# Kernel tuning notes

Hardware: AMD Instinct MI355X
Metric: run time of the kernel (lower is better)

## Reference

```python
import jax, jax.numpy as jnp
import numpy as np

B, T, D = 4, 2048, 1024

def setup_inputs() -> dict:
    key = jax.random.key(0)
    kx, kq, kk, kv = jax.random.split(key, 4)
    lim = 1.0 / np.sqrt(D)
    x = jax.random.normal(kx, (B, T, D), dtype=jnp.float32)
    # nn.Linear weights (stored as [out,in]); applied as x @ W.T
    W_q = jax.random.uniform(kq, (D, D), jnp.float32, -lim, lim)
    W_k = jax.random.uniform(kk, (D, D), jnp.float32, -lim, lim)
    W_v = jax.random.uniform(kv, (D, D), jnp.float32, -lim, lim)
    return {"x": x, "W_q": W_q, "W_k": W_k, "W_v": W_v}

def reference(x, W_q, W_k, W_v):
    d = x.shape[-1]
    Q = jnp.einsum('btd,ed->bte', x, W_q)
    K = jnp.einsum('btd,ed->bte', x, W_k)
    V = jnp.einsum('btd,ed->bte', x, W_v)
    att = jnp.einsum('bqd,bkd->bqk', Q, K) / jnp.sqrt(jnp.asarray(d, x.dtype))
    weights = jax.nn.softmax(att, axis=-1)  # NOTE: original applies no causal mask
    return jnp.einsum('bqk,bkd->bqd', weights, V)
```

## Files before the change

kernel.cpp:

```cpp
#include <hip/hip_runtime.h>
#include <hip/hip_bf16.h>
#include <math.h>
#include <type_traits>


typedef short shortx8 __attribute__((ext_vector_type(8)));
typedef short shortx4 __attribute__((ext_vector_type(4)));
typedef float floatx16 __attribute__((ext_vector_type(16)));
typedef __attribute__((address_space(3))) void lds_void_t;
typedef __attribute__((address_space(1))) const void gmem_void_t;

#define GLD16(gp, lp) \
    __builtin_amdgcn_global_load_lds((gmem_void_t*)(gp), (lds_void_t*)(lp), 16, 0, 0)

#define MODE_PROJ 0
#define MODE_EXP  1
#define MODE_DIV  2

template <int MODE>
__global__ __launch_bounds__(512) void mfma_gemm_abt(
    const __hip_bfloat16* __restrict__ A, const __hip_bfloat16* __restrict__ B,
    void* __restrict__ Cv, float* __restrict__ rowsum,
    __hip_bfloat16* __restrict__ Vt,
    int M, int N, int K, long sA, long sB, long sC, float alpha)
{
    __shared__ __hip_bfloat16 As[256 * 64];
    __shared__ __hip_bfloat16 Bs[128 * 64];

    using CT = std::conditional_t<MODE == MODE_DIV, float, __hip_bfloat16>;

    const int z = blockIdx.z;
    A += (long)z * sA;
    B += (long)z * sB;
    CT* C = (CT*)Cv + (long)z * sC;

    const int t     = threadIdx.x;
    const int wave  = t >> 6;
    const int lane  = t & 63;
    const int m0    = blockIdx.x * 256;
    const int n0    = blockIdx.y * 128;
    const int wm    = (wave >> 1) * 64;
    const int wn    = (wave & 1) * 64;
    const int lrow  = lane & 31;
    const int lhalf = lane >> 5;

    const int srow = t >> 3;
    const int scol = (((t & 7) ^ ((t >> 3) & 7))) * 8;

    const int fr = lrow & 7;

    floatx16 acc[2][2] = {};

    for (int k0 = 0; k0 < K; k0 += 64) {
        #pragma unroll
        for (int q = 0; q < 4; ++q)
            GLD16(A + (long)(m0 + 64 * q + srow) * K + k0 + scol,
                  As + q * 4096 + wave * 512);
        #pragma unroll
        for (int q = 0; q < 2; ++q)
            GLD16(B + (long)(n0 + 64 * q + srow) * K + k0 + scol,
                  Bs + q * 4096 + wave * 512);
        __syncthreads();

        #pragma unroll
        for (int h = 0; h < 4; ++h) {
            const int koff = ((2 * h + lhalf) ^ fr) * 8;
            shortx8 af[2], bf[2];
            #pragma unroll
            for (int i = 0; i < 2; ++i)
                af[i] = *(const shortx8*)(As + (wm + 32 * i + lrow) * 64 + koff);
            #pragma unroll
            for (int j = 0; j < 2; ++j)
                bf[j] = *(const shortx8*)(Bs + (wn + 32 * j + lrow) * 64 + koff);
            #pragma unroll
            for (int i = 0; i < 2; ++i)
                #pragma unroll
                for (int j = 0; j < 2; ++j)
                    acc[i][j] = __builtin_amdgcn_mfma_f32_32x32x16_bf16(
                        af[i], bf[j], acc[i][j], 0, 0, 0);
        }
        __syncthreads();
    }

    if constexpr (MODE == MODE_PROJ) {
        if (z == 2) {
            const int bz   = m0 >> 11;
            const long bo  = (long)bz * N * 2048;
            #pragma unroll
            for (int i = 0; i < 2; ++i)
                #pragma unroll
                for (int j = 0; j < 2; ++j)
                    #pragma unroll
                    for (int g = 0; g < 4; ++g) {
                        const int trow = (m0 + wm + 32 * i + g * 8 + 4 * lhalf) & 2047;
                        const long col = n0 + wn + 32 * j + lrow;
                        shortx4 pk;
                        #pragma unroll
                        for (int r = 0; r < 4; ++r) {
                            __hip_bfloat16 hb = __float2bfloat16(acc[i][j][4 * g + r]);
                            pk[r] = *(short*)&hb;
                        }
                        *(shortx4*)(Vt + bo + col * 2048 + trow) = pk;
                    }
        } else {
            #pragma unroll
            for (int i = 0; i < 2; ++i)
                #pragma unroll
                for (int j = 0; j < 2; ++j)
                    #pragma unroll
                    for (int g = 0; g < 4; ++g)
                        #pragma unroll
                        for (int r = 0; r < 4; ++r) {
                            const long row = m0 + wm + 32 * i + g * 8 + 4 * lhalf + r;
                            const long col = n0 + wn + 32 * j + lrow;
                            C[row * N + col] = __float2bfloat16(acc[i][j][4 * g + r]);
                        }
        }
    } else if constexpr (MODE == MODE_EXP) {
        #pragma unroll
        for (int i = 0; i < 2; ++i) {
            float rs[16];
            #pragma unroll
            for (int reg = 0; reg < 16; ++reg) rs[reg] = 0.0f;
            #pragma unroll
            for (int j = 0; j < 2; ++j)
                #pragma unroll
                for (int g = 0; g < 4; ++g)
                    #pragma unroll
                    for (int r = 0; r < 4; ++r) {
                        const long row = m0 + wm + 32 * i + g * 8 + 4 * lhalf + r;
                        const long col = n0 + wn + 32 * j + lrow;
                        const float e = __expf(acc[i][j][4 * g + r] * alpha);
                        rs[4 * g + r] += e;
                        C[row * N + col] = __float2bfloat16(e);
                    }
            #pragma unroll
            for (int reg = 0; reg < 16; ++reg) {
                float v = rs[reg];
                v += __shfl_xor(v, 1);
                v += __shfl_xor(v, 2);
                v += __shfl_xor(v, 4);
                v += __shfl_xor(v, 8);
                v += __shfl_xor(v, 16);
                if (lrow == 0) {
                    const long row = m0 + wm + 32 * i + (reg >> 2) * 8 + 4 * lhalf + (reg & 3);
                    atomicAdd(&rowsum[(long)z * M + row], v);
                }
            }
        }
    } else {
        #pragma unroll
        for (int i = 0; i < 2; ++i) {
            float inv[16];
            #pragma unroll
            for (int g = 0; g < 4; ++g)
                #pragma unroll
                for (int r = 0; r < 4; ++r) {
                    const long row = m0 + wm + 32 * i + g * 8 + 4 * lhalf + r;
                    inv[4 * g + r] = 1.0f / rowsum[(long)z * M + row];
                }
            #pragma unroll
            for (int j = 0; j < 2; ++j)
                #pragma unroll
                for (int g = 0; g < 4; ++g)
                    #pragma unroll
                    for (int r = 0; r < 4; ++r) {
                        const long row = m0 + wm + 32 * i + g * 8 + 4 * lhalf + r;
                        const long col = n0 + wn + 32 * j + lrow;
                        C[row * N + col] = acc[i][j][4 * g + r] * inv[4 * g + r];
                    }
        }
    }
}

__global__ __launch_bounds__(256) void prep(
    const float* __restrict__ x,
    const float* __restrict__ W0, const float* __restrict__ W1,
    const float* __restrict__ W2,
    __hip_bfloat16* __restrict__ xb, __hip_bfloat16* __restrict__ Wb,
    float* __restrict__ rowsum, int n4x, int n4w)
{
    const long i = (long)blockIdx.x * 256 + threadIdx.x;
    if (i < 2048) {
        float4 zz; zz.x = zz.y = zz.z = zz.w = 0.0f;
        ((float4*)rowsum)[i] = zz;
    }
    const float* src;
    __hip_bfloat16* dst;
    long j;
    if (i < n4x) {
        src = x; dst = xb; j = i;
    } else {
        const long k = i - n4x;
        const int w  = (int)(k >> 18);
        j = k & (n4w - 1);
        src = (w == 0) ? W0 : (w == 1) ? W1 : W2;
        dst = Wb + (long)w * n4w * 4;
    }
    const float4 f = ((const float4*)src)[j];
    dst[j * 4 + 0] = __float2bfloat16(f.x);
    dst[j * 4 + 1] = __float2bfloat16(f.y);
    dst[j * 4 + 2] = __float2bfloat16(f.z);
    dst[j * 4 + 3] = __float2bfloat16(f.w);
}

extern "C" void kernel_launch(void* const* d_in, const int* in_sizes, int n_in,
                              void* d_out, int out_size, void* d_ws, size_t ws_size,
                              hipStream_t stream)
{
    constexpr int  Bb = 4, T = 2048, D = 1024;
    constexpr int  M  = Bb * T;
    constexpr long TD = (long)T * D;
    constexpr long TT = (long)T * T;
    constexpr long MD = (long)M * D;

    const float* x  = (const float*)d_in[0];
    const float* Wq = (const float*)d_in[1];
    const float* Wk = (const float*)d_in[2];
    const float* Wv = (const float*)d_in[3];
    float* out = (float*)d_out;

    __hip_bfloat16* Q  = (__hip_bfloat16*)d_ws;
    __hip_bfloat16* Kb = Q + MD;
    __hip_bfloat16* Vt = Kb + MD;
    __hip_bfloat16* P  = Vt + MD;
    __hip_bfloat16* xb = P + (long)Bb * TT;
    __hip_bfloat16* Wb = xb + MD;
    float*     rowsum  = (float*)(Wb + 3L * D * D);

    constexpr int n4x = (int)(MD / 4);
    constexpr int n4w = D * D / 4;
    prep<<<dim3((n4x + 3 * n4w) / 256), dim3(256), 0, stream>>>(
        x, Wq, Wk, Wv, xb, Wb, rowsum, n4x, n4w);

    dim3 blk(512);

    mfma_gemm_abt<MODE_PROJ><<<dim3(M / 256, D / 128, 3), blk, 0, stream>>>(
        xb, Wb, Q, nullptr, Vt, M, D, D, 0, (long)D * D, MD, 1.0f);

    mfma_gemm_abt<MODE_EXP><<<dim3(T / 256, T / 128, Bb), blk, 0, stream>>>(
        Q, Kb, P, rowsum, nullptr, T, T, D, TD, TD, TT, 0.03125f);

    mfma_gemm_abt<MODE_DIV><<<dim3(T / 256, D / 128, Bb), blk, 0, stream>>>(
        P, Vt, out, rowsum, nullptr, T, D, T, TT, TD, TD, 1.0f);

    (void)in_sizes; (void)n_in; (void)out_size; (void)ws_size;
}
```

Baseline: 250.9 us.

## Triple-buffer LDS with async global-to-LDS prefetch and interleaved MFMA barriers

```diff
diff --git a/kernel.cpp b/kernel.cpp
--- a/kernel.cpp
+++ b/kernel.cpp
@@ -24,8 +24,7 @@
     __hip_bfloat16* __restrict__ Vt,
     int M, int N, int K, long sA, long sB, long sC, float alpha)
 {
-    __shared__ __hip_bfloat16 As[256 * 64];
-    __shared__ __hip_bfloat16 Bs[128 * 64];
+    __shared__ __hip_bfloat16 lds[3 * 24576];
 
     using CT = std::conditional_t<MODE == MODE_DIV, float, __hip_bfloat16>;
 
@@ -46,21 +45,46 @@
 
     const int srow = t >> 3;
     const int scol = (((t & 7) ^ ((t >> 3) & 7))) * 8;
-
-    const int fr = lrow & 7;
+    const int fr   = lrow & 7;
+    const int ldst = wave * 512;
+
+    const long qa = 64L * (long)K;
+    const __hip_bfloat16* Ag = A + (long)(m0 + srow) * K + scol;
+    const __hip_bfloat16* Bg = B + (long)(n0 + srow) * K + scol;
 
     floatx16 acc[2][2] = {};
-
-    for (int k0 = 0; k0 < K; k0 += 64) {
-        #pragma unroll
-        for (int q = 0; q < 4; ++q)
-            GLD16(A + (long)(m0 + 64 * q + srow) * K + k0 + scol,
-                  As + q * 4096 + wave * 512);
-        #pragma unroll
-        for (int q = 0; q < 2; ++q)
-            GLD16(B + (long)(n0 + 64 * q + srow) * K + k0 + scol,
-                  Bs + q * 4096 + wave * 512);
-        __syncthreads();
+    const int KT = K >> 6;
+
+    GLD16(Ag,              lds + ldst);
+    GLD16(Ag + qa,         lds + 4096  + ldst);
+    GLD16(Ag + 2 * qa,     lds + 8192  + ldst);
+    GLD16(Ag + 3 * qa,     lds + 12288 + ldst);
+    GLD16(Bg,              lds + 16384 + ldst);
+    GLD16(Bg + qa,         lds + 20480 + ldst);
+    GLD16(Ag + 64,          lds + 24576 + ldst);
+    GLD16(Ag + 64 + qa,     lds + 24576 + 4096  + ldst);
+    GLD16(Ag + 64 + 2 * qa, lds + 24576 + 8192  + ldst);
+    GLD16(Ag + 64 + 3 * qa, lds + 24576 + 12288 + ldst);
+    GLD16(Bg + 64,          lds + 24576 + 16384 + ldst);
+    GLD16(Bg + 64 + qa,     lds + 24576 + 20480 + ldst);
+
+    const __hip_bfloat16* Apf = Ag + 128;
+    const __hip_bfloat16* Bpf = Bg + 128;
+    int rbuf = 0;
+    int wbuf = 2;
+
+    for (int kt = 0; kt < KT; ++kt) {
+        if (kt == KT - 1) {
+            asm volatile("s_waitcnt vmcnt(0)" ::: "memory");
+        } else {
+            asm volatile("s_waitcnt vmcnt(6)" ::: "memory");
+        }
+        __builtin_amdgcn_s_barrier();
+
+        const __hip_bfloat16* As = lds + rbuf * 24576;
+        const __hip_bfloat16* Bs = As + 16384;
+        __hip_bfloat16*       Lw = (__hip_bfloat16*)lds + wbuf * 24576;
+        const bool pf = (kt + 2) < KT;
 
         #pragma unroll
         for (int h = 0; h < 4; ++h) {
@@ -72,14 +96,35 @@
             #pragma unroll
             for (int j = 0; j < 2; ++j)
                 bf[j] = *(const shortx8*)(Bs + (wn + 32 * j + lrow) * 64 + koff);
+
+            if (pf) {
+                if (h == 0) {
+                    GLD16(Apf,          Lw + ldst);
+                    GLD16(Apf + qa,     Lw + 4096  + ldst);
+                } else if (h == 1) {
+                    GLD16(Apf + 2 * qa, Lw + 8192  + ldst);
+                    GLD16(Apf + 3 * qa, Lw + 12288 + ldst);
+                } else if (h == 2) {
+                    GLD16(Bpf,          Lw + 16384 + ldst);
+                    GLD16(Bpf + qa,     Lw + 20480 + ldst);
+                }
+            }
+
+            __builtin_amdgcn_s_barrier();
+            __builtin_amdgcn_s_setprio(1);
             #pragma unroll
             for (int i = 0; i < 2; ++i)
                 #pragma unroll
                 for (int j = 0; j < 2; ++j)
                     acc[i][j] = __builtin_amdgcn_mfma_f32_32x32x16_bf16(
                         af[i], bf[j], acc[i][j], 0, 0, 0);
-        }
-        __syncthreads();
+            __builtin_amdgcn_s_setprio(0);
+            __builtin_amdgcn_s_barrier();
+        }
+
+        Apf += 64; Bpf += 64;
+        rbuf = (rbuf == 2) ? 0 : rbuf + 1;
+        wbuf = (wbuf == 2) ? 0 : wbuf + 1;
     }
 
     if constexpr (MODE == MODE_PROJ) {
```

New measurement: 263.8 us. +5.1%, slower.

## Double-buffer LDS with async prefetch and enlarge GEMM tile to 256x256

Applied to the files above, without the earlier changes.

```diff
diff --git a/kernel.cpp b/kernel.cpp
--- a/kernel.cpp
+++ b/kernel.cpp
@@ -18,14 +18,13 @@
 #define MODE_DIV  2
 
 template <int MODE>
-__global__ __launch_bounds__(512) void mfma_gemm_abt(
+__global__ __launch_bounds__(512, 2) void mfma_gemm_abt(
     const __hip_bfloat16* __restrict__ A, const __hip_bfloat16* __restrict__ B,
     void* __restrict__ Cv, float* __restrict__ rowsum,
     __hip_bfloat16* __restrict__ Vt,
     int M, int N, int K, long sA, long sB, long sC, float alpha)
 {
-    __shared__ __hip_bfloat16 As[256 * 64];
-    __shared__ __hip_bfloat16 Bs[128 * 64];
+    __shared__ __hip_bfloat16 lds[2 * 32768];
 
     using CT = std::conditional_t<MODE == MODE_DIV, float, __hip_bfloat16>;
 
@@ -38,56 +37,86 @@
     const int wave  = t >> 6;
     const int lane  = t & 63;
     const int m0    = blockIdx.x * 256;
-    const int n0    = blockIdx.y * 128;
-    const int wm    = (wave >> 1) * 64;
-    const int wn    = (wave & 1) * 64;
+    const int n0    = blockIdx.y * 256;
+    const int wm    = (wave >> 2) * 128;
+    const int wn    = (wave & 3) * 64;
     const int lrow  = lane & 31;
     const int lhalf = lane >> 5;
 
-    const int srow = t >> 3;
-    const int scol = (((t & 7) ^ ((t >> 3) & 7))) * 8;
-
-    const int fr = lrow & 7;
-
-    floatx16 acc[2][2] = {};
-
-    for (int k0 = 0; k0 < K; k0 += 64) {
+    const int rb_a  = (wave >> 2) * 8192;
+    const int rb_b  = 16384 + (wave & 3) * 4096;
+    const int rdoff = lrow * 16 + lhalf * 8;
+
+    const long grow = (long)(lane >> 1) * K + ((lane & 1) << 3);
+    const __hip_bfloat16* Ag = A + (long)(m0 + wave * 32) * K + grow;
+    const __hip_bfloat16* Bg = B + (long)(n0 + wave * 32) * K + grow;
+    const int sdst = wave * 2048;
+
+#define STAGE(bb, koff) do {                                              \
+        _Pragma("unroll")                                                 \
+        for (int q = 0; q < 4; ++q)                                       \
+            GLD16(Ag + (koff) + q * 16, lds + (bb) + sdst + q * 512);     \
+        _Pragma("unroll")                                                 \
+        for (int q = 0; q < 4; ++q)                                       \
+            GLD16(Bg + (koff) + q * 16, lds + (bb) + 16384 + sdst + q * 512); \
+    } while (0)
+
+    floatx16 acc[4][2] = {};
+    const int KT = K >> 6;
+
+    STAGE(0, 0);
+
+    for (int kt = 0; kt < KT; ++kt) {
+        const int cur = (kt & 1) << 15;
+        if (kt + 1 < KT) {
+            STAGE(((kt + 1) & 1) << 15, (kt + 1) * 64);
+            asm volatile("s_waitcnt vmcnt(8)" ::: "memory");
+        } else {
+            asm volatile("s_waitcnt vmcnt(0)" ::: "memory");
+        }
+        __builtin_amdgcn_s_barrier();
+        const __hip_bfloat16* Ls = lds + cur;
+
         #pragma unroll
-        for (int q = 0; q < 4; ++q)
-            GLD16(A + (long)(m0 + 64 * q + srow) * K + k0 + scol,
-                  As + q * 4096 + wave * 512);
-        #pragma unroll
-        for (int q = 0; q < 2; ++q)
-            GLD16(B + (long)(n0 + 64 * q + srow) * K + k0 + scol,
-                  Bs + q * 4096 + wave * 512);
-        __syncthreads();
-
-        #pragma unroll
-        for (int h = 0; h < 4; ++h) {
-            const int koff = ((2 * h + lhalf) ^ fr) * 8;
-            shortx8 af[2], bf[2];
-            #pragma unroll
-            for (int i = 0; i < 2; ++i)
-                af[i] = *(const shortx8*)(As + (wm + 32 * i + lrow) * 64 + koff);
-            #pragma unroll
-            for (int j = 0; j < 2; ++j)
-                bf[j] = *(const shortx8*)(Bs + (wn + 32 * j + lrow) * 64 + koff);
-            #pragma unroll
-            for (int i = 0; i < 2; ++i)
+        for (int hh = 0; hh < 2; ++hh) {
+            const int p0 = (2 * hh) * 512 + rdoff;
+            shortx8 a0[4], a1[4], b0[2], b1[2];
+            #pragma unroll
+            for (int i = 0; i < 4; ++i) {
+                a0[i] = *(const shortx8*)(Ls + rb_a + i * 2048 + p0);
+                a1[i] = *(const shortx8*)(Ls + rb_a + i * 2048 + p0 + 512);
+            }
+            #pragma unroll
+            for (int j = 0; j < 2; ++j) {
+                b0[j] = *(const shortx8*)(Ls + rb_b + j * 2048 + p0);
+                b1[j] = *(const shortx8*)(Ls + rb_b + j * 2048 + p0 + 512);
+            }
+            __builtin_amdgcn_s_barrier();
+            __builtin_amdgcn_s_setprio(1);
+            #pragma unroll
+            for (int i = 0; i < 4; ++i)
                 #pragma unroll
                 for (int j = 0; j < 2; ++j)
                     acc[i][j] = __builtin_amdgcn_mfma_f32_32x32x16_bf16(
-                        af[i], bf[j], acc[i][j], 0, 0, 0);
-        }
-        __syncthreads();
-    }
+                        a0[i], b0[j], acc[i][j], 0, 0, 0);
+            #pragma unroll
+            for (int i = 0; i < 4; ++i)
+                #pragma unroll
+                for (int j = 0; j < 2; ++j)
+                    acc[i][j] = __builtin_amdgcn_mfma_f32_32x32x16_bf16(
+                        a1[i], b1[j], acc[i][j], 0, 0, 0);
+            __builtin_amdgcn_s_setprio(0);
+            __builtin_amdgcn_s_barrier();
+        }
+    }
+#undef STAGE
 
     if constexpr (MODE == MODE_PROJ) {
         if (z == 2) {
             const int bz   = m0 >> 11;
             const long bo  = (long)bz * N * 2048;
             #pragma unroll
-            for (int i = 0; i < 2; ++i)
+            for (int i = 0; i < 4; ++i)
                 #pragma unroll
                 for (int j = 0; j < 2; ++j)
                     #pragma unroll
@@ -104,7 +133,7 @@
                     }
         } else {
             #pragma unroll
-            for (int i = 0; i < 2; ++i)
+            for (int i = 0; i < 4; ++i)
                 #pragma unroll
                 for (int j = 0; j < 2; ++j)
                     #pragma unroll
@@ -118,7 +147,7 @@
         }
     } else if constexpr (MODE == MODE_EXP) {
         #pragma unroll
-        for (int i = 0; i < 2; ++i) {
+        for (int i = 0; i < 4; ++i) {
             float rs[16];
             #pragma unroll
             for (int reg = 0; reg < 16; ++reg) rs[reg] = 0.0f;
@@ -150,7 +179,7 @@
         }
     } else {
         #pragma unroll
-        for (int i = 0; i < 2; ++i) {
+        for (int i = 0; i < 4; ++i) {
             float inv[16];
             #pragma unroll
             for (int g = 0; g < 4; ++g)
@@ -235,13 +264,13 @@
 
     dim3 blk(512);
 
-    mfma_gemm_abt<MODE_PROJ><<<dim3(M / 256, D / 128, 3), blk, 0, stream>>>(
+    mfma_gemm_abt<MODE_PROJ><<<dim3(M / 256, D / 256, 3), blk, 0, stream>>>(
         xb, Wb, Q, nullptr, Vt, M, D, D, 0, (long)D * D, MD, 1.0f);
 
-    mfma_gemm_abt<MODE_EXP><<<dim3(T / 256, T / 128, Bb), blk, 0, stream>>>(
+    mfma_gemm_abt<MODE_EXP><<<dim3(T / 256, T / 256, Bb), blk, 0, stream>>>(
         Q, Kb, P, rowsum, nullptr, T, T, D, TD, TD, TT, 0.03125f);
 
-    mfma_gemm_abt<MODE_DIV><<<dim3(T / 256, D / 128, Bb), blk, 0, stream>>>(
+    mfma_gemm_abt<MODE_DIV><<<dim3(T / 256, D / 256, Bb), blk, 0, stream>>>(
         P, Vt, out, rowsum, nullptr, T, D, T, TT, TD, TD, 1.0f);
 
     (void)in_sizes; (void)n_in; (void)out_size; (void)ws_size;
```

Result: slower. 345.7 us (+37.8%).

## Pre-tile operands into MFMA fragment layout and double-buffer LDS staging

Applied to the files above, without the earlier changes.

```diff
diff --git a/kernel.cpp b/kernel.cpp
--- a/kernel.cpp
+++ b/kernel.cpp
@@ -18,14 +18,13 @@
 #define MODE_DIV  2
 
 template <int MODE>
-__global__ __launch_bounds__(512) void mfma_gemm_abt(
+__global__ __launch_bounds__(512, 4) void mfma_gemm_abt(
     const __hip_bfloat16* __restrict__ A, const __hip_bfloat16* __restrict__ B,
     void* __restrict__ Cv, float* __restrict__ rowsum,
     __hip_bfloat16* __restrict__ Vt,
     int M, int N, int K, long sA, long sB, long sC, float alpha)
 {
-    __shared__ __hip_bfloat16 As[256 * 64];
-    __shared__ __hip_bfloat16 Bs[128 * 64];
+    __shared__ __hip_bfloat16 lds[2 * 12288];
 
     using CT = std::conditional_t<MODE == MODE_DIV, float, __hip_bfloat16>;
 
@@ -44,43 +43,62 @@
     const int lrow  = lane & 31;
     const int lhalf = lane >> 5;
 
-    const int srow = t >> 3;
-    const int scol = (((t & 7) ^ ((t >> 3) & 7))) * 8;
-
-    const int fr = lrow & 7;
+    const long KU   = (long)(K >> 4);
+    const long aOff = (long)((m0 >> 5) + wave) * KU * 512 + lane * 8;
+    const long bOff = ((long)((n0 >> 5) + (wave >> 1)) * KU + (wave & 1)) * 512
+                      + lane * 8;
+    const int  dA   = wave * 1024;
+    const int  dB   = 8192 + wave * 512;
+
+    const int raB = (wave >> 1) * 2048 + lane * 8;
+    const int rbB = 8192 + (wave & 1) * 2048 + lane * 8;
+
+#define STAGE(bo_, k2_) do {                                               \
+        GLD16(A + aOff + (long)(k2_) * 512,       lds + (bo_) + dA);       \
+        GLD16(A + aOff + (long)((k2_) + 1) * 512, lds + (bo_) + dA + 512); \
+        GLD16(B + bOff + (long)(k2_) * 512,       lds + (bo_) + dB);       \
+    } while (0)
 
     floatx16 acc[2][2] = {};
-
-    for (int k0 = 0; k0 < K; k0 += 64) {
+    const int KT = K >> 5;
+
+    STAGE(0, 0);
+    asm volatile("s_waitcnt vmcnt(0)" ::: "memory");
+    __builtin_amdgcn_s_barrier();
+
+    for (int kt = 0; kt < KT; ++kt) {
+        if (kt + 1 < KT)
+            STAGE(((kt + 1) & 1) * 12288, 2 * (kt + 1));
+
+        const __hip_bfloat16* Ls = lds + (kt & 1) * 12288;
+
         #pragma unroll
-        for (int q = 0; q < 4; ++q)
-            GLD16(A + (long)(m0 + 64 * q + srow) * K + k0 + scol,
-                  As + q * 4096 + wave * 512);
-        #pragma unroll
-        for (int q = 0; q < 2; ++q)
-            GLD16(B + (long)(n0 + 64 * q + srow) * K + k0 + scol,
-                  Bs + q * 4096 + wave * 512);
-        __syncthreads();
-
-        #pragma unroll
-        for (int h = 0; h < 4; ++h) {
-            const int koff = ((2 * h + lhalf) ^ fr) * 8;
-            shortx8 af[2], bf[2];
-            #pragma unroll
-            for (int i = 0; i < 2; ++i)
-                af[i] = *(const shortx8*)(As + (wm + 32 * i + lrow) * 64 + koff);
+        for (int s = 0; s < 2; ++s) {
+            shortx8 a[2], b[2];
+            #pragma unroll
+            for (int i = 0; i < 2; ++i)
+                a[i] = *(const shortx8*)(Ls + raB + (2 * i + s) * 512);
             #pragma unroll
             for (int j = 0; j < 2; ++j)
-                bf[j] = *(const shortx8*)(Bs + (wn + 32 * j + lrow) * 64 + koff);
+                b[j] = *(const shortx8*)(Ls + rbB + (2 * j + s) * 512);
+            __builtin_amdgcn_s_setprio(1);
             #pragma unroll
             for (int i = 0; i < 2; ++i)
                 #pragma unroll
                 for (int j = 0; j < 2; ++j)
                     acc[i][j] = __builtin_amdgcn_mfma_f32_32x32x16_bf16(
-                        af[i], bf[j], acc[i][j], 0, 0, 0);
-        }
-        __syncthreads();
-    }
+                        a[i], b[j], acc[i][j], 0, 0, 0);
+            __builtin_amdgcn_s_setprio(0);
+        }
+        asm volatile("s_waitcnt vmcnt(0)" ::: "memory");
+        __builtin_amdgcn_s_barrier();
+    }
+#undef STAGE
+
+    auto sidx = [&](int row, int col) -> long {
+        return ((long)(row >> 5) * (N >> 4) + (col >> 4)) * 512
+             + ((row & 31) + 32 * ((col >> 3) & 1)) * 8 + (col & 7);
+    };
 
     if constexpr (MODE == MODE_PROJ) {
         if (z == 2) {
@@ -92,15 +110,18 @@
                 for (int j = 0; j < 2; ++j)
                     #pragma unroll
                     for (int g = 0; g < 4; ++g) {
-                        const int trow = (m0 + wm + 32 * i + g * 8 + 4 * lhalf) & 2047;
-                        const long col = n0 + wn + 32 * j + lrow;
+                        const int t0 = (m0 + wm + 32 * i + g * 8 + 4 * lhalf) & 2047;
+                        const int d  = n0 + wn + 32 * j + lrow;
                         shortx4 pk;
                         #pragma unroll
                         for (int r = 0; r < 4; ++r) {
                             __hip_bfloat16 hb = __float2bfloat16(acc[i][j][4 * g + r]);
                             pk[r] = *(short*)&hb;
                         }
-                        *(shortx4*)(Vt + bo + col * 2048 + trow) = pk;
+                        const long idx = bo
+                            + ((long)(d >> 5) * 128 + (t0 >> 4)) * 512
+                            + ((d & 31) + 32 * ((t0 >> 3) & 1)) * 8 + (t0 & 7);
+                        *(shortx4*)(Vt + idx) = pk;
                     }
         } else {
             #pragma unroll
@@ -111,9 +132,9 @@
                     for (int g = 0; g < 4; ++g)
                         #pragma unroll
                         for (int r = 0; r < 4; ++r) {
-                            const long row = m0 + wm + 32 * i + g * 8 + 4 * lhalf + r;
-                            const long col = n0 + wn + 32 * j + lrow;
-                            C[row * N + col] = __float2bfloat16(acc[i][j][4 * g + r]);
+                            const int row = m0 + wm + 32 * i + g * 8 + 4 * lhalf + r;
+                            const int col = n0 + wn + 32 * j + lrow;
+                            C[sidx(row, col)] = __float2bfloat16(acc[i][j][4 * g + r]);
                         }
         }
     } else if constexpr (MODE == MODE_EXP) {
@@ -128,11 +149,11 @@
                 for (int g = 0; g < 4; ++g)
                     #pragma unroll
                     for (int r = 0; r < 4; ++r) {
-                        const long row = m0 + wm + 32 * i + g * 8 + 4 * lhalf + r;
-                        const long col = n0 + wn + 32 * j + lrow;
+                        const int row = m0 + wm + 32 * i + g * 8 + 4 * lhalf + r;
+                        const int col = n0 + wn + 32 * j + lrow;
                         const float e = __expf(acc[i][j][4 * g + r] * alpha);
                         rs[4 * g + r] += e;
-                        C[row * N + col] = __float2bfloat16(e);
+                        C[sidx(row, col)] = __float2bfloat16(e);
                     }
             #pragma unroll
             for (int reg = 0; reg < 16; ++reg) {
@@ -198,10 +219,16 @@
         dst = Wb + (long)w * n4w * 4;
     }
     const float4 f = ((const float4*)src)[j];
-    dst[j * 4 + 0] = __float2bfloat16(f.x);
-    dst[j * 4 + 1] = __float2bfloat16(f.y);
-    dst[j * 4 + 2] = __float2bfloat16(f.z);
-    dst[j * 4 + 3] = __float2bfloat16(f.w);
+    const int row = (int)(j >> 8);
+    const int k0  = (int)(j & 255) * 4;
+    const long idx = ((long)(row >> 5) * 64 + (k0 >> 4)) * 512
+                   + ((row & 31) + 32 * ((k0 >> 3) & 1)) * 8 + (k0 & 7);
+    shortx4 pk;
+    __hip_bfloat16 h0 = __float2bfloat16(f.x); pk[0] = *(short*)&h0;
+    __hip_bfloat16 h1 = __float2bfloat16(f.y); pk[1] = *(short*)&h1;
+    __hip_bfloat16 h2 = __float2bfloat16(f.z); pk[2] = *(short*)&h2;
+    __hip_bfloat16 h3 = __float2bfloat16(f.w); pk[3] = *(short*)&h3;
+    *(shortx4*)(dst + idx) = pk;
 }
 
 extern "C" void kernel_launch(void* const* d_in, const int* in_sizes, int n_in,
```

Result: slower. 257.0 us (+2.4%).
